# Optimization experiments

Hardware: AMD Instinct MI355X
Metric: run time of the kernel (lower is better)

The kernel has to match this reference:

```python
import jax, jax.numpy as jnp
import numpy as np

ALPHA = 0.2  # LeakyReLU negative slope
NEG_BIG = -9e15


def setup_inputs() -> dict:
    key = jax.random.key(0)
    k1, k2, k3, k4 = jax.random.split(key, 4)
    N, F_IN, F_OUT = 8192, 256, 128
    h = jax.random.normal(k1, (N, F_IN), dtype=jnp.float32)
    adj = jax.random.randint(k2, (N, N), 0, 2, dtype=jnp.int32)
    # xavier_uniform with gain=1.414
    def xavier(k, shape, gain=1.414):
        fan_in, fan_out = shape[0], shape[1]
        bound = gain * np.sqrt(6.0 / (fan_in + fan_out))
        return jax.random.uniform(k, shape, jnp.float32, -bound, bound)
    W = xavier(k3, (F_IN, F_OUT))
    a = xavier(k4, (2 * F_OUT, 1))
    return {"h": h, "adj": adj, "W": W, "a": a}


def reference(h, adj, W, a):
    # Wh: [N, F_out]
    Wh = h @ W
    F_out = W.shape[1]
    a1 = a[:F_out, 0]   # attends to source (row) node
    a2 = a[F_out:, 0]   # attends to target (col) node
    # Additive decomposition of concat([Wh_i, Wh_j]) @ a:
    # e[i, j] = leaky_relu(Wh_i . a1 + Wh_j . a2)
    f1 = Wh @ a1  # [N]
    f2 = Wh @ a2  # [N]
    e = jax.nn.leaky_relu(f1[:, None] + f2[None, :], negative_slope=ALPHA)  # [N, N]
    scores = jnp.where(adj > 0, e, jnp.float32(NEG_BIG))
    attention = jax.nn.softmax(scores, axis=1)
    # dropout is identity in eval mode (training=False)
    h_prime = attention @ Wh  # [N, F_out]
    return h_prime
```

## Files before the change

### kernel.cpp

```cpp
#include <hip/hip_runtime.h>


#define N_NODES 8192
#define F_IN 256
#define F_OUT 128
#define RPB 32
#define JCH 128
#define JSPLIT 2
#define JRANGE (N_NODES / JSPLIT)
#define NCH (JRANGE / JCH)

typedef _Float16 half8 __attribute__((ext_vector_type(8)));
typedef float floatx4 __attribute__((ext_vector_type(4)));
typedef float f32x4 __attribute__((ext_vector_type(4)));

__device__ __align__(16) float g_Wh[N_NODES * F_OUT];
__device__ __align__(16) _Float16 g_WhT[(size_t)F_OUT * N_NODES];
__device__ __align__(16) float g_f1[N_NODES];
__device__ __align__(16) float g_f2[N_NODES];
__device__ __align__(16) float g_part[JSPLIT][N_NODES * F_OUT];
__device__ __align__(16) float g_spart[JSPLIT][N_NODES];

#define GLD16(lds, gp)                                                        \
  __builtin_amdgcn_global_load_lds(                                           \
      (const __attribute__((address_space(1))) unsigned int*)(gp),            \
      (__attribute__((address_space(3))) unsigned int*)(lds), 16, 0, 0)

__global__ __launch_bounds__(256, 2) void wh_kernel(
    const float* __restrict__ h, const float* __restrict__ W) {
  __shared__ float hT[F_IN][20];
  const int t = threadIdx.x;
  const int i0 = blockIdx.x * 16;
  {
    const int row = t >> 4;
    const int fu = t & 15;
#pragma unroll
    for (int r = 0; r < 4; ++r) {
      const int ku = r * 16 + fu;
      const float4 v = *(const float4*)(h + (size_t)(i0 + row) * F_IN + ku * 4);
      hT[ku * 4 + 0][row] = v.x; hT[ku * 4 + 1][row] = v.y;
      hT[ku * 4 + 2][row] = v.z; hT[ku * 4 + 3][row] = v.w;
    }
  }
  __syncthreads();
  const int c = t & 127;
  const int rg = t >> 7;
  float acc[8];
#pragma unroll
  for (int r = 0; r < 8; ++r) acc[r] = 0.f;
#pragma unroll 8
  for (int k = 0; k < F_IN; ++k) {
    const float wv = W[k * F_OUT + c];
    const float4 x0 = *(const float4*)(&hT[k][rg * 8]);
    const float4 x1 = *(const float4*)(&hT[k][rg * 8 + 4]);
    acc[0] = fmaf(x0.x, wv, acc[0]); acc[1] = fmaf(x0.y, wv, acc[1]);
    acc[2] = fmaf(x0.z, wv, acc[2]); acc[3] = fmaf(x0.w, wv, acc[3]);
    acc[4] = fmaf(x1.x, wv, acc[4]); acc[5] = fmaf(x1.y, wv, acc[5]);
    acc[6] = fmaf(x1.z, wv, acc[6]); acc[7] = fmaf(x1.w, wv, acc[7]);
  }
#pragma unroll
  for (int r = 0; r < 8; ++r)
    g_Wh[(size_t)(i0 + rg * 8 + r) * F_OUT + c] = acc[r];
  union { _Float16 hh[8]; uint4 u4; } pk;
#pragma unroll
  for (int r = 0; r < 8; ++r) pk.hh[r] = (_Float16)acc[r];
  *(uint4*)(g_WhT + (size_t)c * N_NODES + i0 + rg * 8) = pk.u4;
}

__global__ __launch_bounds__(256) void f12_kernel(const float* __restrict__ a) {
  const int t = threadIdx.x;
  const int row = blockIdx.x * 2 + (t >> 7);
  const int c = t & 127;
  const float wh = g_Wh[(size_t)row * F_OUT + c];
  float p1 = wh * a[c];
  float p2 = wh * a[F_OUT + c];
  for (int o = 32; o > 0; o >>= 1) {
    p1 += __shfl_down(p1, o, 64);
    p2 += __shfl_down(p2, o, 64);
  }
  __shared__ float s1[4], s2[4];
  const int w = t >> 6;
  if ((t & 63) == 0) { s1[w] = p1; s2[w] = p2; }
  __syncthreads();
  if ((t & 127) == 0) {
    g_f1[row] = s1[w] + s1[w + 1];
    g_f2[row] = s2[w] + s2[w + 1];
  }
}

__device__ __forceinline__ float score_p(int a, float f2v, float f1r) {
  float s = f1r + f2v;
  s = fmaxf(s, 0.2f * s);
  float arg = (a > 0) ? fmaf(s, 1.44269504088896f, -16.0f) : -1.0e5f;
  return __builtin_amdgcn_exp2f(arg);
}

__global__ __launch_bounds__(256, 2) void gat_attn_kernel(const int* __restrict__ adj) {
  const int t = threadIdx.x;
  const int wave = t >> 6;
  const int lane = t & 63;
  const int mrow = lane & 15;
  const int quad = lane >> 4;
  const int i0 = blockIdx.x * RPB;
  const int js = blockIdx.y;
  const int jbase = js * JRANGE;

  __shared__ int ldsAdj[2][RPB * JCH];
  __shared__ float ldsF2[2][256];
  __shared__ float ldsO[RPB][F_OUT];
  __shared__ float ldsS[4][RPB];

  int rm[4], cm[4];
  {
    half8 a1f, b1f, a2f, b2f;
#pragma unroll
    for (int e = 0; e < 8; ++e) {
      a1f[e] = (_Float16)0; b1f[e] = (_Float16)0;
      a2f[e] = (_Float16)0; b2f[e] = (_Float16)0;
    }
    if (quad == 0) {
      a1f[0] = (_Float16)mrow; b1f[0] = (_Float16)1;
      a2f[0] = (_Float16)1;    b2f[0] = (_Float16)mrow;
    }
    floatx4 d1 = (floatx4)0.f, d2 = (floatx4)0.f;
    d1 = __builtin_amdgcn_mfma_f32_16x16x32_f16(a1f, b1f, d1, 0, 0, 0);
    d2 = __builtin_amdgcn_mfma_f32_16x16x32_f16(a2f, b2f, d2, 0, 0, 0);
#pragma unroll
    for (int r = 0; r < 4; ++r) { rm[r] = (int)d1[r]; cm[r] = (int)d2[r]; }
  }

  const float f1r0 = g_f1[i0 + mrow];
  const float f1r1 = g_f1[i0 + 16 + mrow];

  half8 ones;
#pragma unroll
  for (int e = 0; e < 8; ++e) ones[e] = (_Float16)1;

  floatx4 acc[2][8];
  floatx4 asum[2];
#pragma unroll
  for (int tl = 0; tl < 2; ++tl) {
    asum[tl] = (floatx4)0.f;
#pragma unroll
    for (int ct = 0; ct < 8; ++ct) acc[tl][ct] = (floatx4)0.f;
  }

#define DMA(cc, bb) do {                                                      \
    _Pragma("unroll")                                                         \
    for (int R = 0; R < 4; ++R) {                                             \
      const int m = R * 8 + wave * 2 + (lane >> 5);                           \
      const int u = ((lane & 31) - m) & 31;                                   \
      const int* gp = adj + (size_t)(i0 + m) * N_NODES + jbase + (cc) * JCH + u * 4; \
      GLD16(&ldsAdj[bb][(R * 8 + wave * 2) * JCH], gp);                       \
    }                                                                         \
    if (wave == 0) {                                                          \
      int idx = jbase + (cc) * JCH + lane * 4;                                \
      idx = idx > (N_NODES - 4) ? (N_NODES - 4) : idx;                        \
      GLD16(&ldsF2[bb][0], g_f2 + idx);                                       \
    }                                                                         \
  } while (0)

  DMA(0, 0);
  __builtin_amdgcn_s_waitcnt(0);
  __syncthreads();

#pragma unroll 1
  for (int c = 0; c < NCH; ++c) {
    const int b = c & 1;
    const int jloc = wave * 32 + quad * 8;
    const int jglob = jbase + c * JCH + jloc;

    half8 bfr[8];
#pragma unroll
    for (int ct = 0; ct < 8; ++ct)
      bfr[ct] = *(const half8*)(g_WhT + (size_t)(ct * 16 + mrow) * N_NODES + jglob);

    if (c + 1 < NCH) DMA(c + 1, b ^ 1);

    const int u0 = jloc >> 2;
    const char* base = (const char*)&ldsAdj[b][0];
    const int4 A00 = *(const int4*)(base + mrow * 512 + (((u0 + mrow) & 31) << 4));
    const int4 A01 = *(const int4*)(base + mrow * 512 + (((u0 + 1 + mrow) & 31) << 4));
    const int m2 = mrow + 16;
    const int4 A10 = *(const int4*)(base + m2 * 512 + (((u0 + m2) & 31) << 4));
    const int4 A11 = *(const int4*)(base + m2 * 512 + (((u0 + 1 + m2) & 31) << 4));
    const float4 F0 = *(const float4*)&ldsF2[b][jloc];
    const float4 F1 = *(const float4*)&ldsF2[b][jloc + 4];

    half8 af0, af1;
    af0[0] = (_Float16)score_p(A00.x, F0.x, f1r0);
    af0[1] = (_Float16)score_p(A00.y, F0.y, f1r0);
    af0[2] = (_Float16)score_p(A00.z, F0.z, f1r0);
    af0[3] = (_Float16)score_p(A00.w, F0.w, f1r0);
    af0[4] = (_Float16)score_p(A01.x, F1.x, f1r0);
    af0[5] = (_Float16)score_p(A01.y, F1.y, f1r0);
    af0[6] = (_Float16)score_p(A01.z, F1.z, f1r0);
    af0[7] = (_Float16)score_p(A01.w, F1.w, f1r0);
    af1[0] = (_Float16)score_p(A10.x, F0.x, f1r1);
    af1[1] = (_Float16)score_p(A10.y, F0.y, f1r1);
    af1[2] = (_Float16)score_p(A10.z, F0.z, f1r1);
    af1[3] = (_Float16)score_p(A10.w, F0.w, f1r1);
    af1[4] = (_Float16)score_p(A11.x, F1.x, f1r1);
    af1[5] = (_Float16)score_p(A11.y, F1.y, f1r1);
    af1[6] = (_Float16)score_p(A11.z, F1.z, f1r1);
    af1[7] = (_Float16)score_p(A11.w, F1.w, f1r1);

#pragma unroll
    for (int ct = 0; ct < 8; ++ct) {
      acc[0][ct] = __builtin_amdgcn_mfma_f32_16x16x32_f16(af0, bfr[ct], acc[0][ct], 0, 0, 0);
      acc[1][ct] = __builtin_amdgcn_mfma_f32_16x16x32_f16(af1, bfr[ct], acc[1][ct], 0, 0, 0);
    }
    asum[0] = __builtin_amdgcn_mfma_f32_16x16x32_f16(af0, ones, asum[0], 0, 0, 0);
    asum[1] = __builtin_amdgcn_mfma_f32_16x16x32_f16(af1, ones, asum[1], 0, 0, 0);

    __builtin_amdgcn_s_waitcnt(0);
    __syncthreads();
  }
#undef DMA

  if (mrow == 0) {
#pragma unroll
    for (int tl = 0; tl < 2; ++tl)
#pragma unroll
      for (int r = 0; r < 4; ++r)
        ldsS[wave][tl * 16 + rm[r]] = asum[tl][r];
  }
  for (int w = 0; w < 4; ++w) {
    if (wave == w) {
#pragma unroll
      for (int tl = 0; tl < 2; ++tl)
#pragma unroll
        for (int ct = 0; ct < 8; ++ct)
#pragma unroll
          for (int r = 0; r < 4; ++r) {
            float* p = &ldsO[tl * 16 + rm[r]][ct * 16 + cm[r]];
            if (w == 0) *p = acc[tl][ct][r];
            else        *p += acc[tl][ct][r];
          }
    }
    __syncthreads();
  }
  {
    const int row = t >> 3;
    const int c0 = (t & 7) * 16;
    float* dst = g_part[js] + (size_t)(i0 + row) * F_OUT + c0;
#pragma unroll
    for (int q = 0; q < 4; ++q)
      *(f32x4*)(dst + q * 4) = *(const f32x4*)(&ldsO[row][c0 + q * 4]);
    if (t < RPB)
      g_spart[js][i0 + t] = ldsS[0][t] + ldsS[1][t] + ldsS[2][t] + ldsS[3][t];
  }
}

__global__ __launch_bounds__(256) void comb_kernel(float* __restrict__ out) {
  const int u = blockIdx.x * 256 + threadIdx.x;
  const int row = u >> 5;
  const float s = g_spart[0][row] + g_spart[1][row];
  const f32x4 v = ((const f32x4*)g_part[0])[u] + ((const f32x4*)g_part[1])[u];
  ((f32x4*)out)[u] = v * (1.0f / s);
}

extern "C" void kernel_launch(void* const* d_in, const int* in_sizes, int n_in,
                              void* d_out, int out_size, void* d_ws, size_t ws_size,
                              hipStream_t stream) {
  const float* h = (const float*)d_in[0];
  const int* adj = (const int*)d_in[1];
  const float* W = (const float*)d_in[2];
  const float* a = (const float*)d_in[3];
  float* out = (float*)d_out;
  (void)d_ws; (void)ws_size;

  wh_kernel<<<dim3(N_NODES / 16), dim3(256), 0, stream>>>(h, W);
  f12_kernel<<<dim3(N_NODES / 2), dim3(256), 0, stream>>>(a);
  gat_attn_kernel<<<dim3(N_NODES / RPB, JSPLIT), dim3(256), 0, stream>>>(adj);
  comb_kernel<<<dim3(N_NODES * F_OUT / 4 / 256), dim3(256), 0, stream>>>(out);
}
```

Measured before the change: 420.8 us.

## Halve rows per block, split columns four ways, stream adjacency non-temporally

```diff
diff --git a/kernel.cpp b/kernel.cpp
--- a/kernel.cpp
+++ b/kernel.cpp
@@ -4,9 +4,9 @@
 #define N_NODES 8192
 #define F_IN 256
 #define F_OUT 128
-#define RPB 32
+#define RPB 16
 #define JCH 128
-#define JSPLIT 2
+#define JSPLIT 4
 #define JRANGE (N_NODES / JSPLIT)
 #define NCH (JRANGE / JCH)
 
@@ -21,10 +21,10 @@
 __device__ __align__(16) float g_part[JSPLIT][N_NODES * F_OUT];
 __device__ __align__(16) float g_spart[JSPLIT][N_NODES];
 
-#define GLD16(lds, gp)                                                        \
+#define GLD16NT(lds, gp)                                                      \
   __builtin_amdgcn_global_load_lds(                                           \
       (const __attribute__((address_space(1))) unsigned int*)(gp),            \
-      (__attribute__((address_space(3))) unsigned int*)(lds), 16, 0, 0)
+      (__attribute__((address_space(3))) unsigned int*)(lds), 16, 0, 2)
 
 __global__ __launch_bounds__(256, 2) void wh_kernel(
     const float* __restrict__ h, const float* __restrict__ W) {
@@ -95,7 +95,7 @@
   return __builtin_amdgcn_exp2f(arg);
 }
 
-__global__ __launch_bounds__(256, 2) void gat_attn_kernel(const int* __restrict__ adj) {
+__global__ __launch_bounds__(256, 4) void gat_attn_kernel(const int* __restrict__ adj) {
   const int t = threadIdx.x;
   const int wave = t >> 6;
   const int lane = t & 63;
@@ -106,7 +106,6 @@
   const int jbase = js * JRANGE;
 
   __shared__ int ldsAdj[2][RPB * JCH];
-  __shared__ float ldsF2[2][256];
   __shared__ float ldsO[RPB][F_OUT];
   __shared__ float ldsS[4][RPB];
 
@@ -129,124 +128,94 @@
     for (int r = 0; r < 4; ++r) { rm[r] = (int)d1[r]; cm[r] = (int)d2[r]; }
   }
 
-  const float f1r0 = g_f1[i0 + mrow];
-  const float f1r1 = g_f1[i0 + 16 + mrow];
+  const float f1r = g_f1[i0 + mrow];
 
   half8 ones;
 #pragma unroll
   for (int e = 0; e < 8; ++e) ones[e] = (_Float16)1;
 
-  floatx4 acc[2][8];
-  floatx4 asum[2];
-#pragma unroll
-  for (int tl = 0; tl < 2; ++tl) {
-    asum[tl] = (floatx4)0.f;
-#pragma unroll
-    for (int ct = 0; ct < 8; ++ct) acc[tl][ct] = (floatx4)0.f;
-  }
+  floatx4 acc[8];
+  floatx4 asum = (floatx4)0.f;
+#pragma unroll
+  for (int ct = 0; ct < 8; ++ct) acc[ct] = (floatx4)0.f;
 
 #define DMA(cc, bb) do {                                                      \
     _Pragma("unroll")                                                         \
-    for (int R = 0; R < 4; ++R) {                                             \
-      const int m = R * 8 + wave * 2 + (lane >> 5);                           \
+    for (int R = 0; R < 2; ++R) {                                             \
+      const int m0 = wave * 4 + R * 2;                                        \
+      const int m = m0 + (lane >> 5);                                         \
       const int u = ((lane & 31) - m) & 31;                                   \
       const int* gp = adj + (size_t)(i0 + m) * N_NODES + jbase + (cc) * JCH + u * 4; \
-      GLD16(&ldsAdj[bb][(R * 8 + wave * 2) * JCH], gp);                       \
-    }                                                                         \
-    if (wave == 0) {                                                          \
-      int idx = jbase + (cc) * JCH + lane * 4;                                \
-      idx = idx > (N_NODES - 4) ? (N_NODES - 4) : idx;                        \
-      GLD16(&ldsF2[bb][0], g_f2 + idx);                                       \
+      GLD16NT(&ldsAdj[bb][m0 * JCH], gp);                                     \
     }                                                                         \
   } while (0)
 
   DMA(0, 0);
-  __builtin_amdgcn_s_waitcnt(0);
   __syncthreads();
+
+  const int jloc = wave * 32 + quad * 8;
+  const int u0 = jloc >> 2;
 
 #pragma unroll 1
   for (int c = 0; c < NCH; ++c) {
     const int b = c & 1;
-    const int jloc = wave * 32 + quad * 8;
     const int jglob = jbase + c * JCH + jloc;
 
     half8 bfr[8];
 #pragma unroll
     for (int ct = 0; ct < 8; ++ct)
       bfr[ct] = *(const half8*)(g_WhT + (size_t)(ct * 16 + mrow) * N_NODES + jglob);
+    const float4 F0 = *(const float4*)(g_f2 + jglob);
+    const float4 F1 = *(const float4*)(g_f2 + jglob + 4);
 
     if (c + 1 < NCH) DMA(c + 1, b ^ 1);
 
-    const int u0 = jloc >> 2;
     const char* base = (const char*)&ldsAdj[b][0];
-    const int4 A00 = *(const int4*)(base + mrow * 512 + (((u0 + mrow) & 31) << 4));
-    const int4 A01 = *(const int4*)(base + mrow * 512 + (((u0 + 1 + mrow) & 31) << 4));
-    const int m2 = mrow + 16;
-    const int4 A10 = *(const int4*)(base + m2 * 512 + (((u0 + m2) & 31) << 4));
-    const int4 A11 = *(const int4*)(base + m2 * 512 + (((u0 + 1 + m2) & 31) << 4));
-    const float4 F0 = *(const float4*)&ldsF2[b][jloc];
-    const float4 F1 = *(const float4*)&ldsF2[b][jloc + 4];
-
-    half8 af0, af1;
-    af0[0] = (_Float16)score_p(A00.x, F0.x, f1r0);
-    af0[1] = (_Float16)score_p(A00.y, F0.y, f1r0);
-    af0[2] = (_Float16)score_p(A00.z, F0.z, f1r0);
-    af0[3] = (_Float16)score_p(A00.w, F0.w, f1r0);
-    af0[4] = (_Float16)score_p(A01.x, F1.x, f1r0);
-    af0[5] = (_Float16)score_p(A01.y, F1.y, f1r0);
-    af0[6] = (_Float16)score_p(A01.z, F1.z, f1r0);
-    af0[7] = (_Float16)score_p(A01.w, F1.w, f1r0);
-    af1[0] = (_Float16)score_p(A10.x, F0.x, f1r1);
-    af1[1] = (_Float16)score_p(A10.y, F0.y, f1r1);
-    af1[2] = (_Float16)score_p(A10.z, F0.z, f1r1);
-    af1[3] = (_Float16)score_p(A10.w, F0.w, f1r1);
-    af1[4] = (_Float16)score_p(A11.x, F1.x, f1r1);
-    af1[5] = (_Float16)score_p(A11.y, F1.y, f1r1);
-    af1[6] = (_Float16)score_p(A11.z, F1.z, f1r1);
-    af1[7] = (_Float16)score_p(A11.w, F1.w, f1r1);
-
-#pragma unroll
-    for (int ct = 0; ct < 8; ++ct) {
-      acc[0][ct] = __builtin_amdgcn_mfma_f32_16x16x32_f16(af0, bfr[ct], acc[0][ct], 0, 0, 0);
-      acc[1][ct] = __builtin_amdgcn_mfma_f32_16x16x32_f16(af1, bfr[ct], acc[1][ct], 0, 0, 0);
-    }
-    asum[0] = __builtin_amdgcn_mfma_f32_16x16x32_f16(af0, ones, asum[0], 0, 0, 0);
-    asum[1] = __builtin_amdgcn_mfma_f32_16x16x32_f16(af1, ones, asum[1], 0, 0, 0);
-
-    __builtin_amdgcn_s_waitcnt(0);
+    const int4 A0 = *(const int4*)(base + mrow * 512 + (((u0 + mrow) & 31) << 4));
+    const int4 A1 = *(const int4*)(base + mrow * 512 + (((u0 + 1 + mrow) & 31) << 4));
+
+    half8 af;
+    af[0] = (_Float16)score_p(A0.x, F0.x, f1r);
+    af[1] = (_Float16)score_p(A0.y, F0.y, f1r);
+    af[2] = (_Float16)score_p(A0.z, F0.z, f1r);
+    af[3] = (_Float16)score_p(A0.w, F0.w, f1r);
+    af[4] = (_Float16)score_p(A1.x, F1.x, f1r);
+    af[5] = (_Float16)score_p(A1.y, F1.y, f1r);
+    af[6] = (_Float16)score_p(A1.z, F1.z, f1r);
+    af[7] = (_Float16)score_p(A1.w, F1.w, f1r);
+
+#pragma unroll
+    for (int ct = 0; ct < 8; ++ct)
+      acc[ct] = __builtin_amdgcn_mfma_f32_16x16x32_f16(af, bfr[ct], acc[ct], 0, 0, 0);
+    asum = __builtin_amdgcn_mfma_f32_16x16x32_f16(af, ones, asum, 0, 0, 0);
+
     __syncthreads();
   }
 #undef DMA
 
   if (mrow == 0) {
 #pragma unroll
-    for (int tl = 0; tl < 2; ++tl)
-#pragma unroll
-      for (int r = 0; r < 4; ++r)
-        ldsS[wave][tl * 16 + rm[r]] = asum[tl][r];
+    for (int r = 0; r < 4; ++r) ldsS[wave][rm[r]] = asum[r];
   }
   for (int w = 0; w < 4; ++w) {
     if (wave == w) {
 #pragma unroll
-      for (int tl = 0; tl < 2; ++tl)
-#pragma unroll
-        for (int ct = 0; ct < 8; ++ct)
-#pragma unroll
-          for (int r = 0; r < 4; ++r) {
-            float* p = &ldsO[tl * 16 + rm[r]][ct * 16 + cm[r]];
-            if (w == 0) *p = acc[tl][ct][r];
-            else        *p += acc[tl][ct][r];
-          }
+      for (int ct = 0; ct < 8; ++ct)
+#pragma unroll
+        for (int r = 0; r < 4; ++r) {
+          float* p = &ldsO[rm[r]][ct * 16 + cm[r]];
+          if (w == 0) *p = acc[ct][r];
+          else        *p += acc[ct][r];
+        }
     }
     __syncthreads();
   }
   {
-    const int row = t >> 3;
-    const int c0 = (t & 7) * 16;
+    const int row = t >> 4;
+    const int c0 = (t & 15) * 8;
     float* dst = g_part[js] + (size_t)(i0 + row) * F_OUT + c0;
-#pragma unroll
-    for (int q = 0; q < 4; ++q)
-      *(f32x4*)(dst + q * 4) = *(const f32x4*)(&ldsO[row][c0 + q * 4]);
+    *(f32x4*)(dst + 0) = *(const f32x4*)(&ldsO[row][c0 + 0]);
+    *(f32x4*)(dst + 4) = *(const f32x4*)(&ldsO[row][c0 + 4]);
     if (t < RPB)
       g_spart[js][i0 + t] = ldsS[0][t] + ldsS[1][t] + ldsS[2][t] + ldsS[3][t];
   }
@@ -255,8 +224,10 @@
 __global__ __launch_bounds__(256) void comb_kernel(float* __restrict__ out) {
   const int u = blockIdx.x * 256 + threadIdx.x;
   const int row = u >> 5;
-  const float s = g_spart[0][row] + g_spart[1][row];
-  const f32x4 v = ((const f32x4*)g_part[0])[u] + ((const f32x4*)g_part[1])[u];
+  const float s = g_spart[0][row] + g_spart[1][row] +
+                  g_spart[2][row] + g_spart[3][row];
+  const f32x4 v = ((const f32x4*)g_part[0])[u] + ((const f32x4*)g_part[1])[u] +
+                  ((const f32x4*)g_part[2])[u] + ((const f32x4*)g_part[3])[u];
   ((f32x4*)out)[u] = v * (1.0f / s);
 }
 
```

Measured after the change: 477.6 us. 1.14x slower.

## Give each wave private row tiles and adjacency buffers, split columns sixteen ways

Applied to the files above, without the earlier changes.

```diff
diff --git a/kernel.cpp b/kernel.cpp
--- a/kernel.cpp
+++ b/kernel.cpp
@@ -4,9 +4,9 @@
 #define N_NODES 8192
 #define F_IN 256
 #define F_OUT 128
-#define RPB 32
-#define JCH 128
-#define JSPLIT 2
+#define RPB 128
+#define JCH 32
+#define JSPLIT 16
 #define JRANGE (N_NODES / JSPLIT)
 #define NCH (JRANGE / JCH)
 
@@ -21,10 +21,12 @@
 __device__ __align__(16) float g_part[JSPLIT][N_NODES * F_OUT];
 __device__ __align__(16) float g_spart[JSPLIT][N_NODES];
 
-#define GLD16(lds, gp)                                                        \
+#define GLD16NT(lds, gp)                                                      \
   __builtin_amdgcn_global_load_lds(                                           \
       (const __attribute__((address_space(1))) unsigned int*)(gp),            \
-      (__attribute__((address_space(3))) unsigned int*)(lds), 16, 0, 0)
+      (__attribute__((address_space(3))) unsigned int*)(lds), 16, 0, 2)
+
+#define WAITVM14() __builtin_amdgcn_s_waitcnt(0x0F7E)
 
 __global__ __launch_bounds__(256, 2) void wh_kernel(
     const float* __restrict__ h, const float* __restrict__ W) {
@@ -95,7 +97,7 @@
   return __builtin_amdgcn_exp2f(arg);
 }
 
-__global__ __launch_bounds__(256, 2) void gat_attn_kernel(const int* __restrict__ adj) {
+__global__ __launch_bounds__(256, 3) void gat_attn_kernel(const int* __restrict__ adj) {
   const int t = threadIdx.x;
   const int wave = t >> 6;
   const int lane = t & 63;
@@ -104,33 +106,12 @@
   const int i0 = blockIdx.x * RPB;
   const int js = blockIdx.y;
   const int jbase = js * JRANGE;
-
-  __shared__ int ldsAdj[2][RPB * JCH];
-  __shared__ float ldsF2[2][256];
-  __shared__ float ldsO[RPB][F_OUT];
-  __shared__ float ldsS[4][RPB];
-
-  int rm[4], cm[4];
-  {
-    half8 a1f, b1f, a2f, b2f;
-#pragma unroll
-    for (int e = 0; e < 8; ++e) {
-      a1f[e] = (_Float16)0; b1f[e] = (_Float16)0;
-      a2f[e] = (_Float16)0; b2f[e] = (_Float16)0;
-    }
-    if (quad == 0) {
-      a1f[0] = (_Float16)mrow; b1f[0] = (_Float16)1;
-      a2f[0] = (_Float16)1;    b2f[0] = (_Float16)mrow;
-    }
-    floatx4 d1 = (floatx4)0.f, d2 = (floatx4)0.f;
-    d1 = __builtin_amdgcn_mfma_f32_16x16x32_f16(a1f, b1f, d1, 0, 0, 0);
-    d2 = __builtin_amdgcn_mfma_f32_16x16x32_f16(a2f, b2f, d2, 0, 0, 0);
-#pragma unroll
-    for (int r = 0; r < 4; ++r) { rm[r] = (int)d1[r]; cm[r] = (int)d2[r]; }
-  }
-
-  const float f1r0 = g_f1[i0 + mrow];
-  const float f1r1 = g_f1[i0 + 16 + mrow];
+  const int rowbase = i0 + wave * 32;
+
+  __shared__ int ldsAdj[4][2][1024];
+
+  const float f1r0 = g_f1[rowbase + mrow];
+  const float f1r1 = g_f1[rowbase + 16 + mrow];
 
   half8 ones;
 #pragma unroll
@@ -148,44 +129,40 @@
 #define DMA(cc, bb) do {                                                      \
     _Pragma("unroll")                                                         \
     for (int R = 0; R < 4; ++R) {                                             \
-      const int m = R * 8 + wave * 2 + (lane >> 5);                           \
-      const int u = ((lane & 31) - m) & 31;                                   \
-      const int* gp = adj + (size_t)(i0 + m) * N_NODES + jbase + (cc) * JCH + u * 4; \
-      GLD16(&ldsAdj[bb][(R * 8 + wave * 2) * JCH], gp);                       \
-    }                                                                         \
-    if (wave == 0) {                                                          \
-      int idx = jbase + (cc) * JCH + lane * 4;                                \
-      idx = idx > (N_NODES - 4) ? (N_NODES - 4) : idx;                        \
-      GLD16(&ldsF2[bb][0], g_f2 + idx);                                       \
+      const int rr = R * 8 + (lane >> 3);                                     \
+      const int uu = ((lane & 7) - rr) & 7;                                   \
+      const int* gp = adj + (size_t)(rowbase + rr) * N_NODES                  \
+                      + jbase + (cc) * JCH + uu * 4;                          \
+      GLD16NT((char*)&ldsAdj[wave][bb][0] + R * 1024, gp);                    \
     }                                                                         \
   } while (0)
 
   DMA(0, 0);
-  __builtin_amdgcn_s_waitcnt(0);
-  __syncthreads();
 
 #pragma unroll 1
   for (int c = 0; c < NCH; ++c) {
-    const int b = c & 1;
-    const int jloc = wave * 32 + quad * 8;
-    const int jglob = jbase + c * JCH + jloc;
+    const int jglob = jbase + c * JCH + quad * 8;
 
     half8 bfr[8];
 #pragma unroll
     for (int ct = 0; ct < 8; ++ct)
       bfr[ct] = *(const half8*)(g_WhT + (size_t)(ct * 16 + mrow) * N_NODES + jglob);
-
-    if (c + 1 < NCH) DMA(c + 1, b ^ 1);
-
-    const int u0 = jloc >> 2;
-    const char* base = (const char*)&ldsAdj[b][0];
-    const int4 A00 = *(const int4*)(base + mrow * 512 + (((u0 + mrow) & 31) << 4));
-    const int4 A01 = *(const int4*)(base + mrow * 512 + (((u0 + 1 + mrow) & 31) << 4));
-    const int m2 = mrow + 16;
-    const int4 A10 = *(const int4*)(base + m2 * 512 + (((u0 + m2) & 31) << 4));
-    const int4 A11 = *(const int4*)(base + m2 * 512 + (((u0 + 1 + m2) & 31) << 4));
-    const float4 F0 = *(const float4*)&ldsF2[b][jloc];
-    const float4 F1 = *(const float4*)&ldsF2[b][jloc + 4];
+    const float4 F0 = *(const float4*)(g_f2 + jglob);
+    const float4 F1 = *(const float4*)(g_f2 + jglob + 4);
+
+    DMA((c + 1) & (NCH - 1), (c + 1) & 1);
+
+    __builtin_amdgcn_sched_barrier(0);
+    WAITVM14();
+    __builtin_amdgcn_sched_barrier(0);
+
+    const char* wbuf = (const char*)&ldsAdj[wave][c & 1][0];
+    const int s0 = ((quad * 2 + mrow) & 7) * 16;
+    const int s1 = ((quad * 2 + 1 + mrow) & 7) * 16;
+    const int4 A00 = *(const int4*)(wbuf + mrow * 128 + s0);
+    const int4 A01 = *(const int4*)(wbuf + mrow * 128 + s1);
+    const int4 A10 = *(const int4*)(wbuf + (16 + mrow) * 128 + s0);
+    const int4 A11 = *(const int4*)(wbuf + (16 + mrow) * 128 + s1);
 
     half8 af0, af1;
     af0[0] = (_Float16)score_p(A00.x, F0.x, f1r0);
@@ -212,51 +189,49 @@
     }
     asum[0] = __builtin_amdgcn_mfma_f32_16x16x32_f16(af0, ones, asum[0], 0, 0, 0);
     asum[1] = __builtin_amdgcn_mfma_f32_16x16x32_f16(af1, ones, asum[1], 0, 0, 0);
-
-    __builtin_amdgcn_s_waitcnt(0);
-    __syncthreads();
   }
 #undef DMA
 
-  if (mrow == 0) {
-#pragma unroll
-    for (int tl = 0; tl < 2; ++tl)
+  __builtin_amdgcn_s_waitcnt(0);
+  float* stage = (float*)&ldsAdj[wave][0][0];
+  const int orow = lane >> 2;
+  const int cb = lane & 3;
+
+#pragma unroll
+  for (int tl = 0; tl < 2; ++tl) {
+#pragma unroll
+    for (int ct = 0; ct < 8; ++ct)
+#pragma unroll
+      for (int r = 0; r < 4; ++r) {
+        const int ri = quad * 4 + r;
+        stage[ri * 128 + (((ct * 4) + (mrow >> 2) + ri) & 31) * 4 + (mrow & 3)] =
+            acc[tl][ct][r];
+      }
+#pragma unroll
+    for (int q = 0; q < 8; ++q) {
+      const int up = (cb * 8 + q + orow) & 31;
+      const f32x4 v = *(const f32x4*)(stage + orow * 128 + up * 4);
+      *(f32x4*)(g_part[js] + (size_t)(rowbase + tl * 16 + orow) * F_OUT +
+                cb * 32 + q * 4) = v;
+    }
+    if (mrow == 0) {
 #pragma unroll
       for (int r = 0; r < 4; ++r)
-        ldsS[wave][tl * 16 + rm[r]] = asum[tl][r];
-  }
-  for (int w = 0; w < 4; ++w) {
-    if (wave == w) {
-#pragma unroll
-      for (int tl = 0; tl < 2; ++tl)
-#pragma unroll
-        for (int ct = 0; ct < 8; ++ct)
-#pragma unroll
-          for (int r = 0; r < 4; ++r) {
-            float* p = &ldsO[tl * 16 + rm[r]][ct * 16 + cm[r]];
-            if (w == 0) *p = acc[tl][ct][r];
-            else        *p += acc[tl][ct][r];
-          }
-    }
-    __syncthreads();
-  }
-  {
-    const int row = t >> 3;
-    const int c0 = (t & 7) * 16;
-    float* dst = g_part[js] + (size_t)(i0 + row) * F_OUT + c0;
-#pragma unroll
-    for (int q = 0; q < 4; ++q)
-      *(f32x4*)(dst + q * 4) = *(const f32x4*)(&ldsO[row][c0 + q * 4]);
-    if (t < RPB)
-      g_spart[js][i0 + t] = ldsS[0][t] + ldsS[1][t] + ldsS[2][t] + ldsS[3][t];
+        g_spart[js][rowbase + tl * 16 + quad * 4 + r] = asum[tl][r];
+    }
   }
 }
 
 __global__ __launch_bounds__(256) void comb_kernel(float* __restrict__ out) {
   const int u = blockIdx.x * 256 + threadIdx.x;
   const int row = u >> 5;
-  const float s = g_spart[0][row] + g_spart[1][row];
-  const f32x4 v = ((const f32x4*)g_part[0])[u] + ((const f32x4*)g_part[1])[u];
+  float s = 0.f;
+  f32x4 v = (f32x4)0.f;
+#pragma unroll
+  for (int p = 0; p < JSPLIT; ++p) {
+    s += g_spart[p][row];
+    v += ((const f32x4*)g_part[p])[u];
+  }
   ((f32x4*)out)[u] = v * (1.0f / s);
 }
 
```

After: 466.6 us. +10.9%, slower.
